# Kernel tuning notes

Measured on AMD Instinct MI355X. Metric: run time of the kernel, lower is better.

Reference implementation:

```python
import jax, jax.numpy as jnp
import numpy as np

N = 100000
K = 8
DK = 16          # d_in/K == d_out/K
E = 1600000
EPS = 1e-12      # torch F.normalize eps


def setup_inputs() -> dict:
    key = jax.random.key(0)
    k1, k2, k3, k4 = jax.random.split(key, 4)
    f_in = jax.random.normal(k1, (N, K, DK), dtype=jnp.float32)
    Ep = jax.random.randint(k2, (E, 2), 0, N, dtype=jnp.int64)
    En = jax.random.randint(k3, (E, 2), 0, N, dtype=jnp.int64)
    # xavier_uniform over (K, 5*DK, DK): fan_in=5*DK, fan_out=DK
    limit = float(np.sqrt(6.0 / (5 * DK + DK)))
    W = jax.random.uniform(k4, (K, 5 * DK, DK), dtype=jnp.float32,
                           minval=-limit, maxval=limit)
    b = jnp.zeros((1, K, DK), dtype=jnp.float32)
    return {"f_in": f_in, "Ep": Ep, "En": En, "W": W, "b": b}


def _aggregate(Ep, En, f_in):
    n = f_in.shape[0]
    seg = lambda vals, idx: jax.ops.segment_sum(vals, idx, num_segments=n)
    m_p_out = seg(f_in[Ep[:, 1]], Ep[:, 0])
    m_p_in = seg(f_in[Ep[:, 0]], Ep[:, 1])
    m_n_out = seg(f_in[En[:, 1]], En[:, 0])
    m_n_in = seg(f_in[En[:, 0]], En[:, 1])
    return m_p_out, m_p_in, m_n_out, m_n_in


def reference(f_in, Ep, En, W, b):
    m_p_out, m_p_in, m_n_out, m_n_in = _aggregate(Ep, En, f_in)
    # (N, K, 5*DK)
    m_concat = jnp.concatenate([m_p_out, m_p_in, f_in, m_n_out, m_n_in], axis=2)
    # per-factor grouped matmul: (N,K,5DK) x (K,5DK,DK) -> (N,K,DK)
    f_out = jnp.einsum('nkf,kfo->nko', m_concat, W) + b
    a = jnp.tanh(f_out)
    # F.normalize: L2 over dim=1 (factor axis), clamp_min eps
    norm = jnp.maximum(jnp.linalg.norm(a, axis=1, keepdims=True), EPS)
    return a / norm
```

## Files before the change

### kernel.cpp

```cpp
#include <hip/hip_runtime.h>
#include <math.h>


#define ROW 128
#define ROW4 32
#define BC   256
#define BSH  8

__device__ __forceinline__ void push_entry(
    int* __restrict__ cnt, int* __restrict__ ovfCnt, int* __restrict__ ovf,
    int* __restrict__ idxbuf, int seg, int src, int PAD, int ovfCap)
{
    int slot = atomicAdd(&cnt[seg], 1);
    if (slot < PAD) {
        idxbuf[(size_t)seg * PAD + slot] = src;
    } else {
        int oi = atomicAdd(ovfCnt, 1);
        if (oi < ovfCap) { ovf[2*oi] = seg; ovf[2*oi+1] = src; }
    }
}

__global__ __launch_bounds__(256) void fill_kernel(
    const int4* __restrict__ Ep2, const int4* __restrict__ En2,
    const int* __restrict__ Ep, const int* __restrict__ En,
    int* __restrict__ cnt, int* __restrict__ ovfCnt, int* __restrict__ ovf,
    int* __restrict__ idxbuf, int Epairs, int Etail, int N, int PAD, int ovfCap)
{
    int i = blockIdx.x * 256 + threadIdx.x;
    int stride = gridDim.x * 256;
    for (int e = i; e < Epairs; e += stride) {
        int4 p = Ep2[e];
        push_entry(cnt, ovfCnt, ovf, idxbuf, 4*p.x + 0, p.y, PAD, ovfCap);
        push_entry(cnt, ovfCnt, ovf, idxbuf, 4*p.y + 1, p.x, PAD, ovfCap);
        push_entry(cnt, ovfCnt, ovf, idxbuf, 4*p.z + 0, p.w, PAD, ovfCap);
        push_entry(cnt, ovfCnt, ovf, idxbuf, 4*p.w + 1, p.z, PAD, ovfCap);
        int4 q = En2[e];
        push_entry(cnt, ovfCnt, ovf, idxbuf, 4*q.x + 2, q.y, PAD, ovfCap);
        push_entry(cnt, ovfCnt, ovf, idxbuf, 4*q.y + 3, q.x, PAD, ovfCap);
        push_entry(cnt, ovfCnt, ovf, idxbuf, 4*q.z + 2, q.w, PAD, ovfCap);
        push_entry(cnt, ovfCnt, ovf, idxbuf, 4*q.w + 3, q.z, PAD, ovfCap);
    }
    if (i == 0 && Etail) {
        int e = 2 * Epairs;
        int a = Ep[2*e], b = Ep[2*e+1];
        push_entry(cnt, ovfCnt, ovf, idxbuf, 4*a + 0, b, PAD, ovfCap);
        push_entry(cnt, ovfCnt, ovf, idxbuf, 4*b + 1, a, PAD, ovfCap);
        int c = En[2*e], d = En[2*e+1];
        push_entry(cnt, ovfCnt, ovf, idxbuf, 4*c + 2, d, PAD, ovfCap);
        push_entry(cnt, ovfCnt, ovf, idxbuf, 4*d + 3, c, PAD, ovfCap);
    }
}

__global__ __launch_bounds__(256) void fill_bucket(
    const int4* __restrict__ Ep2, const int4* __restrict__ En2,
    const int* __restrict__ Ep, const int* __restrict__ En,
    int* __restrict__ cnt2, int* __restrict__ cells,
    int* __restrict__ ovfCnt, int* __restrict__ ovf,
    int Epairs, int Etail, int B, int CAP, int ovfCap)
{
    __shared__ int lcnt[1024];
    const int w = blockIdx.x;
    int* __restrict__ mycell = cells + (size_t)w * B * CAP;

    for (int i = threadIdx.x; i < 1024; i += 256) lcnt[i] = 0;
    __syncthreads();

    auto pushB = [&](int dst, int l, int src) {
        int bkt  = dst >> BSH;
        int slot = atomicAdd(&lcnt[bkt], 1);
        if (slot < CAP) {
            mycell[(size_t)bkt * CAP + slot] =
                src | ((dst & (BC - 1)) << 17) | (l << 25);
        } else {
            int oi = atomicAdd(ovfCnt, 1);
            if (oi < ovfCap) { ovf[2*oi] = 4*dst + l; ovf[2*oi+1] = src; }
        }
    };

    int stride = gridDim.x * 256;
    for (int e = blockIdx.x * 256 + threadIdx.x; e < Epairs; e += stride) {
        int4 p = Ep2[e];
        pushB(p.x, 0, p.y); pushB(p.y, 1, p.x);
        pushB(p.z, 0, p.w); pushB(p.w, 1, p.z);
        int4 q = En2[e];
        pushB(q.x, 2, q.y); pushB(q.y, 3, q.x);
        pushB(q.z, 2, q.w); pushB(q.w, 3, q.z);
    }
    if (w == 0 && threadIdx.x == 0 && Etail) {
        int e = 2 * Epairs;
        int a = Ep[2*e], b = Ep[2*e+1];
        pushB(a, 0, b); pushB(b, 1, a);
        int c = En[2*e], d = En[2*e+1];
        pushB(c, 2, d); pushB(d, 3, c);
    }
    __syncthreads();
    for (int b = threadIdx.x; b < B; b += 256) {
        int v = lcnt[b];
        cnt2[(size_t)w * B + b] = (v < CAP) ? v : CAP;
    }
}

__global__ __launch_bounds__(512) void build_csr(
    const int* __restrict__ cnt2, const int* __restrict__ cells,
    int* __restrict__ cnt, int* __restrict__ idxbuf,
    int* __restrict__ ovfCnt, int* __restrict__ ovf,
    int N, int B, int CAP, int PAD, int wn, int ovfCap)
{
    __shared__ int scnt[4 * BC];
    const int b     = blockIdx.x >> 1;
    const int hf    = blockIdx.x & 1;
    const int HP    = PAD >> 1;
    const int halfW = wn >> 1;
    const int nodeBase = b << BSH;

    for (int i = threadIdx.x; i < 4 * BC; i += 512) scnt[i] = 0;
    __syncthreads();

    auto proc = [&](int p) {
        int src  = p & 0x1FFFF;
        int dl   = (p >> 17) & (BC - 1);
        int l    = (p >> 25) & 3;
        int segl = (dl << 2) | l;
        int slot = atomicAdd(&scnt[segl], 1);
        int seg  = (nodeBase + dl) * 4 + l;
        if (slot < HP) {
            idxbuf[(size_t)seg * PAD + hf * HP + slot] = src;
        } else {
            int oi = atomicAdd(ovfCnt, 1);
            if (oi < ovfCap) { ovf[2*oi] = seg; ovf[2*oi+1] = src; }
        }
    };

    const int wEnd = (hf + 1) * halfW;
    for (int w = hf * halfW + threadIdx.x; w < wEnd; w += 512) {
        int c = cnt2[(size_t)w * B + b];
        const int4* __restrict__ cell4 =
            (const int4*)(cells + ((size_t)w * B + b) * CAP);
        for (int i = 0; i < c; i += 4) {
            int4 v = cell4[i >> 2];
            proc(v.x);
            if (i + 1 < c) proc(v.y);
            if (i + 2 < c) proc(v.z);
            if (i + 3 < c) proc(v.w);
        }
    }
    __syncthreads();
    for (int i = threadIdx.x; i < 4 * BC; i += 512) {
        int node = nodeBase + (i >> 2);
        if (node < N)
            cnt[(((size_t)node * 4 + (i & 3)) << 1) + hf] = scnt[i];
    }
}

__global__ __launch_bounds__(256) void ovf_kernel(
    const float* __restrict__ f_in, const float* __restrict__ W,
    const int* __restrict__ ovfCnt, const int* __restrict__ ovf,
    float* __restrict__ out, int N, int ovfCap)
{
    const int t = threadIdx.x & 127;
    const int k = t >> 4;
    const int o = t & 15;
    int nOv = *ovfCnt;
    if (nOv > ovfCap) nOv = ovfCap;
    const int group  = blockIdx.x * 2 + (threadIdx.x >> 7);
    const int stride = gridDim.x * 2;
    for (int i = group; i < nOv; i += stride) {
        int seg = ovf[2*i], src = ovf[2*i+1];
        int l = seg & 3;
        int dst = seg >> 2;
        int s = (l < 2) ? l : l + 1;
        float y = 0.f;
#pragma unroll
        for (int ii = 0; ii < 16; ++ii)
            y += f_in[(size_t)src*ROW + k*16 + ii] * W[k*1280 + (s*16 + ii)*16 + o];
        unsafeAtomicAdd(&out[(size_t)dst*ROW + t], y);
    }
}

__global__ __launch_bounds__(256, 4) void pull_kernel(
    const float4* __restrict__ f_in4,
    const float*  __restrict__ f_in,
    const int*    __restrict__ cnt,
    const int*    __restrict__ idxbuf,
    const float*  __restrict__ W,
    const float*  __restrict__ bias,
    const int*    __restrict__ ovfCnt,
    float*        __restrict__ out,
    int N, int PAD, int SPLIT)
{
    __shared__ float4 sacc4[2][5][ROW4];
    __shared__ float  syp[2][ROW];
    __shared__ float  sa[ROW];

    const int tid  = threadIdx.x;
    const int elem = tid & 127;
    const int h    = tid >> 7;
    const int k    = elem >> 4;
    const int o    = elem & 15;
    const int oct  = tid >> 5;
    const int l    = oct >> 1;
    const int hh   = oct & 1;
    const int e4   = tid & 31;
    const int slot = (l < 2) ? l : l + 1;
    const int HP   = PAD >> 1;

    float w[5][8];
#pragma unroll
    for (int s = 0; s < 5; ++s)
#pragma unroll
        for (int i = 0; i < 8; ++i)
            w[s][i] = W[k*1280 + (s*16 + h*8 + i)*16 + o];
    const float bb = bias[elem];
    const int haveOvf = *ovfCnt;

    for (int n = blockIdx.x; n < N; n += gridDim.x) {
        float pre = (h == 0 && haveOvf) ? out[(size_t)n*ROW + elem] : 0.f;

        int j, end;
        size_t base;
        if (SPLIT) {
            int c = cnt[(((size_t)4*n + l) << 1) + hh];
            if (c > HP) c = HP;
            base = (size_t)(4*n + l) * PAD + (size_t)hh * HP;
            j = 0; end = c;
        } else {
            int c = cnt[4*n + l];
            if (c > PAD) c = PAD;
            base = (size_t)(4*n + l) * PAD;
            int mid = (c + 1) >> 1;
            j   = hh ? mid : 0;
            end = hh ? c   : mid;
        }

        float4 acc = make_float4(0.f, 0.f, 0.f, 0.f);
        for (; j + 3 < end; j += 4) {
            int j0 = idxbuf[base + j],     j1 = idxbuf[base + j + 1];
            int j2 = idxbuf[base + j + 2], j3 = idxbuf[base + j + 3];
            float4 r0 = f_in4[(size_t)j0*ROW4 + e4];
            float4 r1 = f_in4[(size_t)j1*ROW4 + e4];
            float4 r2 = f_in4[(size_t)j2*ROW4 + e4];
            float4 r3 = f_in4[(size_t)j3*ROW4 + e4];
            acc.x += r0.x + r1.x + r2.x + r3.x;
            acc.y += r0.y + r1.y + r2.y + r3.y;
            acc.z += r0.z + r1.z + r2.z + r3.z;
            acc.w += r0.w + r1.w + r2.w + r3.w;
        }
        for (; j < end; ++j) {
            float4 r = f_in4[(size_t)idxbuf[base + j]*ROW4 + e4];
            acc.x += r.x; acc.y += r.y; acc.z += r.z; acc.w += r.w;
        }
        sacc4[hh][slot][e4] = acc;
        if (oct == 0) sacc4[0][2][e4] = f_in4[(size_t)n*ROW4 + e4];
        if (oct == 1) sacc4[1][2][e4] = make_float4(0.f, 0.f, 0.f, 0.f);
        __syncthreads();

        float y = 0.f;
#pragma unroll
        for (int s = 0; s < 5; ++s) {
            const float* m0 = (const float*)&sacc4[0][s][0] + k*16 + h*8;
            const float* m1 = (const float*)&sacc4[1][s][0] + k*16 + h*8;
#pragma unroll
            for (int i = 0; i < 8; ++i)
                y += (m0[i] + m1[i]) * w[s][i];
        }
        syp[h][elem] = y;
        __syncthreads();

        float a = 0.f;
        if (h == 0) {
            a = tanhf(syp[0][elem] + syp[1][elem] + bb + pre);
            sa[elem] = a;
        }
        __syncthreads();
        if (h == 0) {
            float ss = 0.f;
#pragma unroll
            for (int k2 = 0; k2 < 8; ++k2) {
                float v = sa[k2*16 + o];
                ss += v * v;
            }
            out[(size_t)n*ROW + elem] = a / fmaxf(sqrtf(ss), 1e-12f);
        }
        __syncthreads();
    }
}

extern "C" void kernel_launch(void* const* d_in, const int* in_sizes, int n_in,
                              void* d_out, int out_size, void* d_ws, size_t ws_size,
                              hipStream_t stream) {
    const float* f_in = (const float*)d_in[0];
    const int*   Ep   = (const int*)d_in[1];
    const int*   En   = (const int*)d_in[2];
    const float* W    = (const float*)d_in[3];
    const float* b    = (const float*)d_in[4];
    float* out = (float*)d_out;

    const int N = in_sizes[0] / ROW;
    const int E = in_sizes[1] / 2;
    const int Epairs = E / 2;
    const int Etail  = E & 1;
    const int M = 4 * N;
    const int B = (N + BC - 1) / BC;

    bool newpath = (N <= 131072) && (B <= 1024);
    int PAD = 0, CAP = 0, WN = 0;
    if (newpath) {
        const int cfg1k[][2] = {{64,48},{48,40},{48,32},{40,32},{40,24},
                                {32,24},{32,16},{24,16},{16,16}};
        const int cfg512[][2] = {{64,48},{56,48},{48,48},{48,40},{40,40},
                                 {40,32},{32,32},{32,24},{24,24},{24,16},
                                 {16,16}};
        const int wnl[2] = {1024, 512};
        for (int wi = 0; wi < 2 && !WN; ++wi) {
            int wn = wnl[wi];
            const int (*cfg)[2] = wi ? cfg512 : cfg1k;
            int ncfg = wi ? 11 : 9;
            for (int i = 0; i < ncfg; ++i) {
                int pad = cfg[i][0], cap = cfg[i][1];
                size_t need = ((size_t)2*M + 64 + (size_t)wn * B
                               + (size_t)M * pad
                               + (size_t)wn * B * cap) * sizeof(int)
                              + 512 * 1024;
                if (need <= ws_size) { PAD = pad; CAP = cap; WN = wn; break; }
            }
        }
        if (!WN) newpath = false;
    }

    if (newpath) {
        int* cnt    = (int*)d_ws;
        int* ovfCnt = cnt + (size_t)2*M;
        int* cnt2   = ovfCnt + 64;
        int* idxbuf = cnt2 + (size_t)WN * B;
        int* cells  = idxbuf + (size_t)M * PAD;
        int* ovf    = cells + (size_t)WN * B * CAP;
        size_t used = ((size_t)2*M + 64 + (size_t)WN * B
                       + (size_t)M * PAD + (size_t)WN * B * CAP) * sizeof(int);
        size_t left = ws_size - used;
        size_t ovfCapSz = left / (2 * sizeof(int));
        int ovfCap = (int)(ovfCapSz > (size_t)(1 << 22) ? (1 << 22) : ovfCapSz);
        if (ovfCap < 1) ovfCap = 1;

        hipMemsetAsync(ovfCnt, 0, 64 * sizeof(int), stream);
        hipMemsetAsync(out, 0, (size_t)out_size * sizeof(float), stream);

        fill_bucket<<<WN, 256, 0, stream>>>((const int4*)Ep, (const int4*)En,
                                            Ep, En, cnt2, cells, ovfCnt, ovf,
                                            Epairs, Etail, B, CAP, ovfCap);
        build_csr<<<2*B, 512, 0, stream>>>(cnt2, cells, cnt, idxbuf,
                                           ovfCnt, ovf, N, B, CAP, PAD, WN,
                                           ovfCap);
        ovf_kernel<<<256, 256, 0, stream>>>(f_in, W, ovfCnt, ovf, out, N, ovfCap);
        pull_kernel<<<8192, 256, 0, stream>>>((const float4*)f_in, f_in, cnt,
                                              idxbuf, W, b, ovfCnt, out, N,
                                              PAD, 1);
        return;
    }

    int PADf = 72;
    size_t fixed;
    do {
        PADf -= 8;
        fixed = ((size_t)M + 64 + (size_t)M * PADf) * sizeof(int);
    } while (PADf > 8 && fixed + 512 * 1024 > ws_size);
    size_t left = (ws_size > fixed) ? (ws_size - fixed) : 8;
    size_t ovfCapSz = left / (2 * sizeof(int));
    int ovfCap = (int)(ovfCapSz > (size_t)(1 << 22) ? (1 << 22) : ovfCapSz);
    if (ovfCap < 1) ovfCap = 1;

    int* cnt    = (int*)d_ws;
    int* ovfCnt = cnt + M;
    int* idxbuf = ovfCnt + 64;
    int* ovf    = idxbuf + (size_t)M * PADf;

    hipMemsetAsync(cnt, 0, ((size_t)M + 64) * sizeof(int), stream);
    hipMemsetAsync(out, 0, (size_t)out_size * sizeof(float), stream);

    fill_kernel<<<2048, 256, 0, stream>>>((const int4*)Ep, (const int4*)En,
                                          Ep, En, cnt, ovfCnt, ovf, idxbuf,
                                          Epairs, Etail, N, PADf, ovfCap);
    ovf_kernel<<<64, 256, 0, stream>>>(f_in, W, ovfCnt, ovf, out, N, ovfCap);
    pull_kernel<<<8192, 256, 0, stream>>>((const float4*)f_in, f_in, cnt,
                                          idxbuf, W, b, ovfCnt, out, N,
                                          PADf, 0);
}
```

Measured before the change: 814.1 us.

## Drop full output memset via overflow node flags, unsplit CSR build, split pull launch

Replaces the full memset of the output with a per-node flag array: a new kernel zeroes only the output rows and sets flags for nodes that receive overflow contributions, and the pull kernel reads the prior partial sum only when the flag is set. The CSR build goes from two half-blocks per bucket, each owning half of every segment's slots, to one block per bucket with a single slot range, which cuts cnt storage to one entry per segment. The padding and capacity config tables are retuned, and the pull kernel is launched twice over node halves. This saves a large memset write, at the cost of an extra small kernel and launch, plus reduced build_csr parallelism and more per-block atomic contention.

```diff
diff --git a/kernel.cpp b/kernel.cpp
--- a/kernel.cpp
+++ b/kernel.cpp
@@ -104,13 +104,10 @@
     const int* __restrict__ cnt2, const int* __restrict__ cells,
     int* __restrict__ cnt, int* __restrict__ idxbuf,
     int* __restrict__ ovfCnt, int* __restrict__ ovf,
-    int N, int B, int CAP, int PAD, int wn, int ovfCap)
+    int N, int B, int CAP, int PAD, int WN, int ovfCap)
 {
     __shared__ int scnt[4 * BC];
-    const int b     = blockIdx.x >> 1;
-    const int hf    = blockIdx.x & 1;
-    const int HP    = PAD >> 1;
-    const int halfW = wn >> 1;
+    const int b = blockIdx.x;
     const int nodeBase = b << BSH;
 
     for (int i = threadIdx.x; i < 4 * BC; i += 512) scnt[i] = 0;
@@ -122,17 +119,17 @@
         int l    = (p >> 25) & 3;
         int segl = (dl << 2) | l;
         int slot = atomicAdd(&scnt[segl], 1);
-        int seg  = (nodeBase + dl) * 4 + l;
-        if (slot < HP) {
-            idxbuf[(size_t)seg * PAD + hf * HP + slot] = src;
+        if (slot < PAD) {
+            idxbuf[(size_t)((nodeBase + dl) * 4 + l) * PAD + slot] = src;
         } else {
             int oi = atomicAdd(ovfCnt, 1);
-            if (oi < ovfCap) { ovf[2*oi] = seg; ovf[2*oi+1] = src; }
+            if (oi < ovfCap) {
+                ovf[2*oi] = (nodeBase + dl) * 4 + l; ovf[2*oi+1] = src;
+            }
         }
     };
 
-    const int wEnd = (hf + 1) * halfW;
-    for (int w = hf * halfW + threadIdx.x; w < wEnd; w += 512) {
+    for (int w = threadIdx.x; w < WN; w += 512) {
         int c = cnt2[(size_t)w * B + b];
         const int4* __restrict__ cell4 =
             (const int4*)(cells + ((size_t)w * B + b) * CAP);
@@ -147,8 +144,21 @@
     __syncthreads();
     for (int i = threadIdx.x; i < 4 * BC; i += 512) {
         int node = nodeBase + (i >> 2);
-        if (node < N)
-            cnt[(((size_t)node * 4 + (i & 3)) << 1) + hf] = scnt[i];
+        if (node < N) cnt[node * 4 + (i & 3)] = scnt[i];
+    }
+}
+
+__global__ __launch_bounds__(128) void ovf_zero(
+    const int* __restrict__ ovfCnt, const int* __restrict__ ovf,
+    float* __restrict__ out, int* __restrict__ nflag, int ovfCap)
+{
+    const int t = threadIdx.x;
+    int nOv = *ovfCnt;
+    if (nOv > ovfCap) nOv = ovfCap;
+    for (int i = blockIdx.x; i < nOv; i += gridDim.x) {
+        int dst = ovf[2*i] >> 2;
+        out[(size_t)dst*ROW + t] = 0.f;
+        if (t == 0) nflag[dst] = 1;
     }
 }
 
@@ -185,8 +195,9 @@
     const float*  __restrict__ W,
     const float*  __restrict__ bias,
     const int*    __restrict__ ovfCnt,
+    const int*    __restrict__ nflag,
     float*        __restrict__ out,
-    int N, int PAD, int SPLIT)
+    int nStart, int nEnd, int PAD)
 {
     __shared__ float4 sacc4[2][5][ROW4];
     __shared__ float  syp[2][ROW];
@@ -202,7 +213,6 @@
     const int hh   = oct & 1;
     const int e4   = tid & 31;
     const int slot = (l < 2) ? l : l + 1;
-    const int HP   = PAD >> 1;
 
     float w[5][8];
 #pragma unroll
@@ -213,24 +223,17 @@
     const float bb = bias[elem];
     const int haveOvf = *ovfCnt;
 
-    for (int n = blockIdx.x; n < N; n += gridDim.x) {
-        float pre = (h == 0 && haveOvf) ? out[(size_t)n*ROW + elem] : 0.f;
-
-        int j, end;
-        size_t base;
-        if (SPLIT) {
-            int c = cnt[(((size_t)4*n + l) << 1) + hh];
-            if (c > HP) c = HP;
-            base = (size_t)(4*n + l) * PAD + (size_t)hh * HP;
-            j = 0; end = c;
-        } else {
-            int c = cnt[4*n + l];
-            if (c > PAD) c = PAD;
-            base = (size_t)(4*n + l) * PAD;
-            int mid = (c + 1) >> 1;
-            j   = hh ? mid : 0;
-            end = hh ? c   : mid;
-        }
+    for (int n = nStart + blockIdx.x; n < nEnd; n += gridDim.x) {
+        float pre = 0.f;
+        if (h == 0 && haveOvf)
+            pre = nflag[n] ? out[(size_t)n*ROW + elem] : 0.f;
+
+        int c = cnt[4*n + l];
+        if (c > PAD) c = PAD;
+        const size_t base = (size_t)(4*n + l) * PAD;
+        const int mid = (c + 1) >> 1;
+        int j         = hh ? mid : 0;
+        const int end = hh ? c   : mid;
 
         float4 acc = make_float4(0.f, 0.f, 0.f, 0.f);
         for (; j + 3 < end; j += 4) {
@@ -301,23 +304,23 @@
     const int Etail  = E & 1;
     const int M = 4 * N;
     const int B = (N + BC - 1) / BC;
+    const int Nh = N >> 1;
 
     bool newpath = (N <= 131072) && (B <= 1024);
     int PAD = 0, CAP = 0, WN = 0;
     if (newpath) {
-        const int cfg1k[][2] = {{64,48},{48,40},{48,32},{40,32},{40,24},
-                                {32,24},{32,16},{24,16},{16,16}};
-        const int cfg512[][2] = {{64,48},{56,48},{48,48},{48,40},{40,40},
-                                 {40,32},{32,32},{32,24},{24,24},{24,16},
-                                 {16,16}};
+        const int cfg1k[][2]  = {{48,32},{40,32},{32,32},{32,24},{24,24},
+                                 {24,16},{16,16}};
+        const int cfg512[][2] = {{64,48},{48,48},{48,40},{40,40},{40,32},
+                                 {32,32},{32,24},{24,24},{16,16}};
         const int wnl[2] = {1024, 512};
         for (int wi = 0; wi < 2 && !WN; ++wi) {
             int wn = wnl[wi];
             const int (*cfg)[2] = wi ? cfg512 : cfg1k;
-            int ncfg = wi ? 11 : 9;
+            int ncfg = wi ? 9 : 7;
             for (int i = 0; i < ncfg; ++i) {
                 int pad = cfg[i][0], cap = cfg[i][1];
-                size_t need = ((size_t)2*M + 64 + (size_t)wn * B
+                size_t need = ((size_t)M + 64 + N + (size_t)wn * B
                                + (size_t)M * pad
                                + (size_t)wn * B * cap) * sizeof(int)
                               + 512 * 1024;
@@ -329,31 +332,36 @@
 
     if (newpath) {
         int* cnt    = (int*)d_ws;
-        int* ovfCnt = cnt + (size_t)2*M;
-        int* cnt2   = ovfCnt + 64;
+        int* ovfCnt = cnt + M;
+        int* nflag  = ovfCnt + 64;
+        int* cnt2   = nflag + N;
         int* idxbuf = cnt2 + (size_t)WN * B;
         int* cells  = idxbuf + (size_t)M * PAD;
         int* ovf    = cells + (size_t)WN * B * CAP;
-        size_t used = ((size_t)2*M + 64 + (size_t)WN * B
+        size_t used = ((size_t)M + 64 + N + (size_t)WN * B
                        + (size_t)M * PAD + (size_t)WN * B * CAP) * sizeof(int);
         size_t left = ws_size - used;
         size_t ovfCapSz = left / (2 * sizeof(int));
         int ovfCap = (int)(ovfCapSz > (size_t)(1 << 22) ? (1 << 22) : ovfCapSz);
         if (ovfCap < 1) ovfCap = 1;
 
-        hipMemsetAsync(ovfCnt, 0, 64 * sizeof(int), stream);
-        hipMemsetAsync(out, 0, (size_t)out_size * sizeof(float), stream);
+        hipMemsetAsync(ovfCnt, 0, ((size_t)64 + N) * sizeof(int), stream);
 
         fill_bucket<<<WN, 256, 0, stream>>>((const int4*)Ep, (const int4*)En,
                                             Ep, En, cnt2, cells, ovfCnt, ovf,
                                             Epairs, Etail, B, CAP, ovfCap);
-        build_csr<<<2*B, 512, 0, stream>>>(cnt2, cells, cnt, idxbuf,
-                                           ovfCnt, ovf, N, B, CAP, PAD, WN,
-                                           ovfCap);
-        ovf_kernel<<<256, 256, 0, stream>>>(f_in, W, ovfCnt, ovf, out, N, ovfCap);
+        build_csr<<<B, 512, 0, stream>>>(cnt2, cells, cnt, idxbuf,
+                                         ovfCnt, ovf, N, B, CAP, PAD, WN,
+                                         ovfCap);
+        ovf_zero<<<256, 128, 0, stream>>>(ovfCnt, ovf, out, nflag, ovfCap);
+        ovf_kernel<<<256, 256, 0, stream>>>(f_in, W, ovfCnt, ovf, out, N,
+                                            ovfCap);
         pull_kernel<<<8192, 256, 0, stream>>>((const float4*)f_in, f_in, cnt,
-                                              idxbuf, W, b, ovfCnt, out, N,
-                                              PAD, 1);
+                                              idxbuf, W, b, ovfCnt, nflag,
+                                              out, 0, Nh, PAD);
+        pull_kernel<<<8192, 256, 0, stream>>>((const float4*)f_in, f_in, cnt,
+                                              idxbuf, W, b, ovfCnt, nflag,
+                                              out, Nh, N, PAD);
         return;
     }
 
@@ -361,7 +369,7 @@
     size_t fixed;
     do {
         PADf -= 8;
-        fixed = ((size_t)M + 64 + (size_t)M * PADf) * sizeof(int);
+        fixed = ((size_t)M + 64 + N + (size_t)M * PADf) * sizeof(int);
     } while (PADf > 8 && fixed + 512 * 1024 > ws_size);
     size_t left = (ws_size > fixed) ? (ws_size - fixed) : 8;
     size_t ovfCapSz = left / (2 * sizeof(int));
@@ -370,17 +378,18 @@
 
     int* cnt    = (int*)d_ws;
     int* ovfCnt = cnt + M;
-    int* idxbuf = ovfCnt + 64;
+    int* nflag  = ovfCnt + 64;
+    int* idxbuf = nflag + N;
     int* ovf    = idxbuf + (size_t)M * PADf;
 
-    hipMemsetAsync(cnt, 0, ((size_t)M + 64) * sizeof(int), stream);
-    hipMemsetAsync(out, 0, (size_t)out_size * sizeof(float), stream);
+    hipMemsetAsync(cnt, 0, ((size_t)M + 64 + N) * sizeof(int), stream);
 
     fill_kernel<<<2048, 256, 0, stream>>>((const int4*)Ep, (const int4*)En,
                                           Ep, En, cnt, ovfCnt, ovf, idxbuf,
                                           Epairs, Etail, N, PADf, ovfCap);
-    ovf_kernel<<<64, 256, 0, stream>>>(f_in, W, ovfCnt, ovf, out, N, ovfCap);
+    ovf_zero<<<256, 128, 0, stream>>>(ovfCnt, ovf, out, nflag, ovfCap);
+    ovf_kernel<<<256, 256, 0, stream>>>(f_in, W, ovfCnt, ovf, out, N, ovfCap);
     pull_kernel<<<8192, 256, 0, stream>>>((const float4*)f_in, f_in, cnt,
-                                          idxbuf, W, b, ovfCnt, out, N,
-                                          PADf, 0);
-}
+                                          idxbuf, W, b, ovfCnt, nflag,
+                                          out, 0, N, PADf);
+}
```

New measurement: 779.4 us. 1.04x faster.
